# Performance work log

Measured on AMD Instinct MI355X. Metric: run time of the kernel, lower is better.

Reference implementation:

```python
import jax, jax.numpy as jnp
import numpy as np

H = 128          # num_hidden
NUM_IN = 256     # 2*H: h_E (H) + gathered neighbor h_V (H)
SCALE = 30.0
LN_EPS = 1e-5


def _ln(x, g, b):
    mu = jnp.mean(x, axis=-1, keepdims=True)
    var = jnp.mean((x - mu) ** 2, axis=-1, keepdims=True)
    return (x - mu) * jax.lax.rsqrt(var + LN_EPS) * g + b


def _gather_nodes(nodes, idx):
    # nodes: [B,L,C], idx: [B,L,K] -> [B,L,K,C]
    B = nodes.shape[0]
    return nodes[jnp.arange(B)[:, None, None], idx]


def _mlp3(x, W1, b1, W2, b2, W3, b3):
    h = jax.nn.gelu(x @ W1 + b1, approximate=False)
    h = jax.nn.gelu(h @ W2 + b2, approximate=False)
    return h @ W3 + b3


def setup_inputs() -> dict:
    key = jax.random.key(0)
    ks = jax.random.split(key, 16)
    B, L, K = 2, 2048, 48
    s = 0.02
    inp = {
        "h_V": jax.random.normal(ks[0], (B, L, H), jnp.float32),
        "h_E": jax.random.normal(ks[1], (B, L, K, H), jnp.float32),
        "E_idx": jax.random.randint(ks[2], (B, L, K), 0, L, jnp.int32),
        "mask_V": jnp.ones((B, L), jnp.float32),
        "mask_attend": jnp.ones((B, L, K), jnp.float32),
        # node-update MLP
        "W1": jax.random.normal(ks[3], (H + NUM_IN, H), jnp.float32) * s,
        "b1": jnp.zeros((H,), jnp.float32),
        "W2": jax.random.normal(ks[4], (H, H), jnp.float32) * s,
        "b2": jnp.zeros((H,), jnp.float32),
        "W3": jax.random.normal(ks[5], (H, H), jnp.float32) * s,
        "b3": jnp.zeros((H,), jnp.float32),
        # edge-update MLP
        "W11": jax.random.normal(ks[6], (H + NUM_IN, H), jnp.float32) * s,
        "b11": jnp.zeros((H,), jnp.float32),
        "W12": jax.random.normal(ks[7], (H, H), jnp.float32) * s,
        "b12": jnp.zeros((H,), jnp.float32),
        "W13": jax.random.normal(ks[8], (H, H), jnp.float32) * s,
        "b13": jnp.zeros((H,), jnp.float32),
        # position-wise FFN (H -> 4H -> H)
        "Win": jax.random.normal(ks[9], (H, 4 * H), jnp.float32) * s,
        "bin": jnp.zeros((4 * H,), jnp.float32),
        "Wout": jax.random.normal(ks[10], (4 * H, H), jnp.float32) * s,
        "bout": jnp.zeros((H,), jnp.float32),
        # LayerNorms
        "g1": jnp.ones((H,), jnp.float32), "be1": jnp.zeros((H,), jnp.float32),
        "g2": jnp.ones((H,), jnp.float32), "be2": jnp.zeros((H,), jnp.float32),
        "g3": jnp.ones((H,), jnp.float32), "be3": jnp.zeros((H,), jnp.float32),
    }
    return inp


def reference(h_V, h_E, E_idx, mask_V, mask_attend,
              W1, b1, W2, b2, W3, b3,
              W11, b11, W12, b12, W13, b13,
              Win, bin, Wout, bout,
              g1, be1, g2, be2, g3, be3):
    K = h_E.shape[-2]
    # --- node update: gather, concat, 3-layer MLP, masked mean-sum, LN residual ---
    h_nbr = _gather_nodes(h_V, E_idx)                               # [B,L,K,H]
    h_V_exp = jnp.broadcast_to(h_V[:, :, None, :], h_nbr.shape)     # [B,L,K,H]
    h_EV = jnp.concatenate([h_V_exp, h_E, h_nbr], axis=-1)          # [B,L,K,3H]
    h_msg = _mlp3(h_EV, W1, b1, W2, b2, W3, b3)                     # [B,L,K,H]
    h_msg = mask_attend[..., None] * h_msg
    dh = jnp.sum(h_msg, axis=-2) / SCALE                            # [B,L,H]
    h_V = _ln(h_V + dh, g1, be1)
    # position-wise FFN + LN residual
    dh = jax.nn.gelu(h_V @ Win + bin, approximate=False) @ Wout + bout
    h_V = _ln(h_V + dh, g2, be2)
    h_V = mask_V[..., None] * h_V
    # --- edge update ---
    h_nbr = _gather_nodes(h_V, E_idx)
    h_V_exp = jnp.broadcast_to(h_V[:, :, None, :], h_nbr.shape)
    h_EV = jnp.concatenate([h_V_exp, h_E, h_nbr], axis=-1)
    h_msg = _mlp3(h_EV, W11, b11, W12, b12, W13, b13)
    h_E = _ln(h_E + h_msg, g3, be3)
    return (h_V, h_E)
```

## Files before the change

kernel.cpp:

```cpp
#include <hip/hip_runtime.h>
#include <hip/hip_bf16.h>

typedef __attribute__((ext_vector_type(8))) short short8;
typedef __attribute__((ext_vector_type(4))) float f32x4;

__device__ inline short f2bf(float f) {
    unsigned u = __builtin_bit_cast(unsigned, f);
    u += 0x7fffu + ((u >> 16) & 1u);
    return (short)(u >> 16);
}
__device__ inline float bf2f(short s) {
    return __builtin_bit_cast(float, ((unsigned)(unsigned short)s) << 16);
}
__device__ inline float bflo(unsigned u) { return __builtin_bit_cast(float, u << 16); }
__device__ inline float bfhi(unsigned u) { return __builtin_bit_cast(float, u & 0xffff0000u); }
__device__ inline unsigned cvt_pk_bf16(float a, float b) {
    unsigned r;
    asm("v_cvt_pk_bf16_f32 %0, %1, %2" : "=v"(r) : "v"(a), "v"(b));
    return r;
}
__device__ inline float gelu_fast(float x) {
    float z = x * (1.0f + 0.044715f * x * x);
    float e = __expf(1.5957691216f * z);
    return x - x * __builtin_amdgcn_rcpf(e + 1.0f);
}
__device__ inline float wred(float s) {
#pragma unroll
    for (int o = 32; o; o >>= 1) s += __shfl_xor(s, o, 64);
    return s;
}

__global__ void pack_all_kernel(const float* __restrict__ W1, const float* __restrict__ W2,
                                const float* __restrict__ W3, const float* __restrict__ W11,
                                const float* __restrict__ W12, const float* __restrict__ W13,
                                const float* __restrict__ Win, const float* __restrict__ Wout,
                                short* __restrict__ out) {
    int b = blockIdx.x;
    if (b < 80) {
        int which = b >> 3;
        const float* Ws[10] = {W1 + 128 * 128, W2, W3, W11 + 128 * 128, W12, W13,
                               W1, W1 + 256 * 128, W11, W11 + 256 * 128};
        const float* W = Ws[which];
        int i = (b & 7) * 256 + threadIdx.x;
        int lane = i & 63, tile = i >> 6;
        int kt = tile & 3, nt = tile >> 2;
        int n = nt * 16 + (lane & 15);
        int k0 = kt * 32 + (lane >> 4) * 8;
        short8 v;
#pragma unroll
        for (int j = 0; j < 8; ++j) v[j] = f2bf(W[(size_t)(k0 + j) * 128 + n]);
        *(short8*)(out + (size_t)which * 16384 + (size_t)i * 8) = v;
    } else if (b < 112) {
        int i = (b - 80) * 256 + threadIdx.x;
        int lane = i & 63, tile = i >> 6;
        int kt = tile & 3, nt = tile >> 2;
        int n = nt * 16 + (lane & 15);
        int k0 = kt * 32 + (lane >> 4) * 8;
        short8 v;
#pragma unroll
        for (int j = 0; j < 8; ++j) v[j] = f2bf(Win[(size_t)(k0 + j) * 512 + n]);
        *(short8*)(out + 163840 + (size_t)i * 8) = v;
    } else {
        int i = (b - 112) * 256 + threadIdx.x;
        int lane = i & 63, tile = i >> 6;
        int kt = tile & 15, nt = tile >> 4;
        int n = nt * 16 + (lane & 15);
        int k0 = kt * 32 + (lane >> 4) * 8;
        short8 v;
#pragma unroll
        for (int j = 0; j < 8; ++j) v[j] = f2bf(Wout[(size_t)(k0 + j) * 128 + n]);
        *(short8*)(out + 229376 + (size_t)i * 8) = v;
    }
}

__global__ __launch_bounds__(256) void node_pre_kernel(
    const float* __restrict__ hV, const short8* __restrict__ Bs,
    const short8* __restrict__ Bn, const float* __restrict__ bias,
    float* __restrict__ Ys, short* __restrict__ Yn) {
    int n0 = blockIdx.x * 16;
    int tid = threadIdx.x, lane = tid & 63, w = tid >> 6;
    __shared__ __align__(16) short A_sw[16 * 128];
    {
        int off = tid * 8;
        int r = off >> 7, c0 = off & 127;
        const float* src = hV + (size_t)n0 * 128 + off;
        float4 f0 = *(const float4*)(src);
        float4 f1 = *(const float4*)(src + 4);
        uint4 u;
        u.x = cvt_pk_bf16(f0.x, f0.y); u.y = cvt_pk_bf16(f0.z, f0.w);
        u.z = cvt_pk_bf16(f1.x, f1.y); u.w = cvt_pk_bf16(f1.z, f1.w);
        *(uint4*)((char*)A_sw + r * 256 + ((c0 * 2) ^ ((r & 7) << 4))) = u;
    }
    __syncthreads();
    const short8* Bp = (w < 2) ? Bs : Bn;
    f32x4 acc[4];
#pragma unroll
    for (int n2 = 0; n2 < 4; ++n2) acc[n2] = (f32x4){0.f, 0.f, 0.f, 0.f};
#pragma unroll
    for (int kt = 0; kt < 4; ++kt) {
        int row = lane & 15;
        int kb = (kt * 32 + (lane >> 4) * 8) * 2;
        short8 a = *(const short8*)((const char*)A_sw + row * 256 + (kb ^ ((row & 7) << 4)));
#pragma unroll
        for (int n2 = 0; n2 < 4; ++n2) {
            int ntl = (w & 1) * 4 + n2;
            short8 bf = Bp[(ntl * 4 + kt) * 64 + lane];
            acc[n2] = __builtin_amdgcn_mfma_f32_16x16x32_bf16(a, bf, acc[n2], 0, 0, 0);
        }
    }
    if (w < 2) {
#pragma unroll
        for (int n2 = 0; n2 < 4; ++n2) {
            int col = ((w & 1) * 4 + n2) * 16 + (lane & 15);
            float bv = bias[col];
#pragma unroll
            for (int i = 0; i < 4; ++i) {
                int row = (lane >> 4) * 4 + i;
                Ys[(size_t)(n0 + row) * 128 + col] = acc[n2][i] + bv;
            }
        }
    } else {
#pragma unroll
        for (int n2 = 0; n2 < 4; ++n2) {
            int col = ((w & 1) * 4 + n2) * 16 + (lane & 15);
#pragma unroll
            for (int i = 0; i < 4; ++i) {
                int row = (lane >> 4) * 4 + i;
                Yn[(size_t)(n0 + row) * 128 + col] = f2bf(acc[n2][i]);
            }
        }
    }
}


__device__ inline void gemm48_a(const short* A_sw, const short8* __restrict__ Wp,
                                int w, int lane, f32x4 acc[3][2]) {
#pragma unroll
    for (int mt = 0; mt < 3; ++mt)
#pragma unroll
        for (int n2 = 0; n2 < 2; ++n2) acc[mt][n2] = (f32x4){0.f, 0.f, 0.f, 0.f};
#pragma unroll
    for (int kt = 0; kt < 4; ++kt) {
        short8 a[3];
        int kb = (kt * 32 + (lane >> 4) * 8) * 2;
#pragma unroll
        for (int mt = 0; mt < 3; ++mt) {
            int row = mt * 16 + (lane & 15);
            a[mt] = *(const short8*)((const char*)A_sw + row * 256 + (kb ^ ((row & 7) << 4)));
        }
#pragma unroll
        for (int n2 = 0; n2 < 2; ++n2) {
            short8 bf = Wp[((w * 2 + n2) * 4 + kt) * 64 + lane];
#pragma unroll
            for (int mt = 0; mt < 3; ++mt)
                acc[mt][n2] = __builtin_amdgcn_mfma_f32_16x16x32_bf16(a[mt], bf, acc[mt][n2], 0, 0, 0);
        }
    }
}

__device__ inline void gemm48_swz(const short* A_sw, const short8* __restrict__ Wp,
                                  int w, int lane, f32x4 acc[2][3]) {
#pragma unroll
    for (int m2 = 0; m2 < 2; ++m2)
#pragma unroll
        for (int nt = 0; nt < 3; ++nt) acc[m2][nt] = (f32x4){0.f, 0.f, 0.f, 0.f};
#pragma unroll
    for (int kt = 0; kt < 4; ++kt) {
        int kb = (kt * 32 + (lane >> 4) * 8) * 2;
        short8 e[3];
#pragma unroll
        for (int nt = 0; nt < 3; ++nt) {
            int row = nt * 16 + (lane & 15);
            e[nt] = *(const short8*)((const char*)A_sw + row * 256 + (kb ^ ((row & 7) << 4)));
        }
#pragma unroll
        for (int m2 = 0; m2 < 2; ++m2) {
            short8 wf = Wp[((w * 2 + m2) * 4 + kt) * 64 + lane];
#pragma unroll
            for (int nt = 0; nt < 3; ++nt)
                acc[m2][nt] = __builtin_amdgcn_mfma_f32_16x16x32_bf16(wf, e[nt], acc[m2][nt], 0, 0, 0);
        }
    }
}

__device__ inline void stage_hE(const float* __restrict__ Eb, short* A_sw, int tid) {
#pragma unroll
    for (int i = 0; i < 3; ++i) {
        int e = tid + i * 256;
        int r = e >> 4, c0 = (e & 15) * 8;
        float4 f0 = *(const float4*)(Eb + r * 128 + c0);
        float4 f1 = *(const float4*)(Eb + r * 128 + c0 + 4);
        uint4 u;
        u.x = cvt_pk_bf16(f0.x, f0.y); u.y = cvt_pk_bf16(f0.z, f0.w);
        u.z = cvt_pk_bf16(f1.x, f1.y); u.w = cvt_pk_bf16(f1.z, f1.w);
        *(uint4*)((char*)A_sw + r * 256 + ((c0 * 2) ^ ((r & 7) << 4))) = u;
    }
}

__device__ inline void epi_l1_reg(f32x4 acc[2][3], const float4 ysv[2],
                                  const uint2 ynv[3][2], short* A_sw, int w, int lane) {
#pragma unroll
    for (int m2 = 0; m2 < 2; ++m2) {
        int featb = (w * 2 + m2) * 16 + ((lane >> 4) << 2);
#pragma unroll
        for (int nt = 0; nt < 3; ++nt) {
            int edge = nt * 16 + (lane & 15);
            uint2 yv = ynv[nt][m2];
            float v0 = gelu_fast(acc[m2][nt][0] + ysv[m2].x + bflo(yv.x));
            float v1 = gelu_fast(acc[m2][nt][1] + ysv[m2].y + bfhi(yv.x));
            float v2 = gelu_fast(acc[m2][nt][2] + ysv[m2].z + bflo(yv.y));
            float v3 = gelu_fast(acc[m2][nt][3] + ysv[m2].w + bfhi(yv.y));
            uint2 pk = {cvt_pk_bf16(v0, v1), cvt_pk_bf16(v2, v3)};
            *(uint2*)((char*)A_sw + edge * 256 + ((featb * 2) ^ ((edge & 7) << 4))) = pk;
        }
    }
}

__device__ inline void epi_l2(f32x4 acc[2][3], const float* __restrict__ b,
                              short* A_sw, int w, int lane) {
#pragma unroll
    for (int m2 = 0; m2 < 2; ++m2) {
        int featb = (w * 2 + m2) * 16 + ((lane >> 4) << 2);
        float b0 = b[featb], b1 = b[featb + 1], b2v = b[featb + 2], b3v = b[featb + 3];
#pragma unroll
        for (int nt = 0; nt < 3; ++nt) {
            int edge = nt * 16 + (lane & 15);
            float v0 = gelu_fast(acc[m2][nt][0] + b0);
            float v1 = gelu_fast(acc[m2][nt][1] + b1);
            float v2 = gelu_fast(acc[m2][nt][2] + b2v);
            float v3 = gelu_fast(acc[m2][nt][3] + b3v);
            uint2 pk = {cvt_pk_bf16(v0, v1), cvt_pk_bf16(v2, v3)};
            *(uint2*)((char*)A_sw + edge * 256 + ((featb * 2) ^ ((edge & 7) << 4))) = pk;
        }
    }
}

__global__ __launch_bounds__(256) void node_msg_kernel(
    const float* __restrict__ hV, const float* __restrict__ hE,
    const int* __restrict__ Eidx, const float* __restrict__ maskAtt,
    const short8* __restrict__ W1bp, const short8* __restrict__ W2p,
    const short8* __restrict__ W3p, const float* __restrict__ b2,
    const float* __restrict__ b3, const float* __restrict__ Ysg,
    const short* __restrict__ Yng, const float* __restrict__ g1,
    const float* __restrict__ be1, float* __restrict__ hv1out) {
    const int node = blockIdx.x;
    const int bb = node >> 11;
    const int tid = threadIdx.x;
    const int lane = tid & 63, w = tid >> 6;

    __shared__ __align__(16) short A_sw[48 * 128];
    __shared__ float mask_s[48];
    __shared__ float red[8];

    const int e0 = lane & 15;
    int featb0 = (w * 2) * 16 + ((lane >> 4) << 2);
    int featb1 = featb0 + 16;
    uint2 ynv[3][2];
    float4 ysv[2];
    {
        int i0 = Eidx[node * 48 + e0];
        int i1 = Eidx[node * 48 + 16 + e0];
        int i2 = Eidx[node * 48 + 32 + e0];
        const short* Y0 = Yng + ((size_t)bb * 2048 + i0) * 128;
        const short* Y1 = Yng + ((size_t)bb * 2048 + i1) * 128;
        const short* Y2 = Yng + ((size_t)bb * 2048 + i2) * 128;
        ynv[0][0] = *(const uint2*)(Y0 + featb0); ynv[0][1] = *(const uint2*)(Y0 + featb1);
        ynv[1][0] = *(const uint2*)(Y1 + featb0); ynv[1][1] = *(const uint2*)(Y1 + featb1);
        ynv[2][0] = *(const uint2*)(Y2 + featb0); ynv[2][1] = *(const uint2*)(Y2 + featb1);
        ysv[0] = *(const float4*)(Ysg + (size_t)node * 128 + featb0);
        ysv[1] = *(const float4*)(Ysg + (size_t)node * 128 + featb1);
    }
    stage_hE(hE + (size_t)node * 6144, A_sw, tid);
    if (tid < 48) mask_s[tid] = maskAtt[node * 48 + tid];
    __syncthreads();

    f32x4 acc[2][3];
    gemm48_swz(A_sw, W1bp, w, lane, acc);
    __syncthreads();
    epi_l1_reg(acc, ysv, ynv, A_sw, w, lane);
    __syncthreads();
    gemm48_swz(A_sw, W2p, w, lane, acc);
    __syncthreads();
    epi_l2(acc, b2, A_sw, w, lane);
    __syncthreads();

    f32x4 acc3[3][2];
    gemm48_a(A_sw, W3p, w, lane, acc3);
    float u[2];
#pragma unroll
    for (int n2 = 0; n2 < 2; ++n2) {
        int col = (w * 2 + n2) * 16 + (lane & 15);
        float b3c = b3[col];
        float s = 0.f;
#pragma unroll
        for (int mt = 0; mt < 3; ++mt)
#pragma unroll
            for (int i = 0; i < 4; ++i) {
                int row = mt * 16 + (lane >> 4) * 4 + i;
                s += (acc3[mt][n2][i] + b3c) * mask_s[row];
            }
        s += __shfl_xor(s, 16, 64);
        s += __shfl_xor(s, 32, 64);
        u[n2] = hV[(size_t)node * 128 + col] + s * (1.0f / 30.0f);
    }
    float ps = wred(u[0] + u[1]) * 0.25f;
    float pq = wred(u[0] * u[0] + u[1] * u[1]) * 0.25f;
    if (lane == 0) { red[w] = ps; red[4 + w] = pq; }
    __syncthreads();
    float S = red[0] + red[1] + red[2] + red[3];
    float Q = red[4] + red[5] + red[6] + red[7];
    float mu = S * (1.0f / 128.0f);
    float var = Q * (1.0f / 128.0f) - mu * mu;
    float rs = rsqrtf(var + 1e-5f);
    if ((lane >> 4) == 0) {
#pragma unroll
        for (int n2 = 0; n2 < 2; ++n2) {
            int col = (w * 2 + n2) * 16 + (lane & 15);
            hv1out[(size_t)node * 128 + col] = (u[n2] - mu) * rs * g1[col] + be1[col];
        }
    }
}

__global__ __launch_bounds__(256) void ffn_kernel(
    const float* __restrict__ hv1, const short8* __restrict__ Winp,
    const float* __restrict__ binp, const short8* __restrict__ Woutp,
    const float* __restrict__ bout, const float* __restrict__ g2,
    const float* __restrict__ be2, const float* __restrict__ maskV,
    float* __restrict__ hVout) {
    int n0 = blockIdx.x * 16;
    int tid = threadIdx.x, lane = tid & 63, w = tid >> 6;
    __shared__ float X[16 * 128];
    __shared__ __align__(16) short A_sw[16 * 128];
    __shared__ __align__(16) short H_sw[16 * 512];

    {
        int off = tid * 8;
        int r = off >> 7, c0 = off & 127;
        const float* src = hv1 + (size_t)n0 * 128 + off;
        float4 f0 = *(const float4*)(src);
        float4 f1 = *(const float4*)(src + 4);
        *(float4*)(&X[off]) = f0;
        *(float4*)(&X[off + 4]) = f1;
        uint4 u;
        u.x = cvt_pk_bf16(f0.x, f0.y); u.y = cvt_pk_bf16(f0.z, f0.w);
        u.z = cvt_pk_bf16(f1.x, f1.y); u.w = cvt_pk_bf16(f1.z, f1.w);
        *(uint4*)((char*)A_sw + r * 256 + ((c0 * 2) ^ ((r & 7) << 4))) = u;
    }
    __syncthreads();

    f32x4 acc1[8];
#pragma unroll
    for (int n2 = 0; n2 < 8; ++n2) acc1[n2] = (f32x4){0.f, 0.f, 0.f, 0.f};
#pragma unroll
    for (int kt = 0; kt < 4; ++kt) {
        int row = lane & 15;
        int kb = (kt * 32 + (lane >> 4) * 8) * 2;
        short8 a = *(const short8*)((const char*)A_sw + row * 256 + (kb ^ ((row & 7) << 4)));
#pragma unroll
        for (int n2 = 0; n2 < 8; ++n2) {
            short8 bf = Winp[((w * 8 + n2) * 4 + kt) * 64 + lane];
            acc1[n2] = __builtin_amdgcn_mfma_f32_16x16x32_bf16(a, bf, acc1[n2], 0, 0, 0);
        }
    }
#pragma unroll
    for (int n2 = 0; n2 < 8; ++n2) {
        int col = (w * 8 + n2) * 16 + (lane & 15);
        float bv = binp[col];
#pragma unroll
        for (int i = 0; i < 4; ++i) {
            int row = (lane >> 4) * 4 + i;
            float v = gelu_fast(acc1[n2][i] + bv);
            *(short*)((char*)H_sw + row * 1024 + ((col * 2) ^ ((row & 7) << 4))) = f2bf(v);
        }
    }
    __syncthreads();

    f32x4 acc2[2];
    acc2[0] = (f32x4){0.f, 0.f, 0.f, 0.f};
    acc2[1] = (f32x4){0.f, 0.f, 0.f, 0.f};
#pragma unroll
    for (int kt = 0; kt < 16; ++kt) {
        int row = lane & 15;
        int kb = (kt * 32 + (lane >> 4) * 8) * 2;
        short8 a = *(const short8*)((const char*)H_sw + row * 1024 + (kb ^ ((row & 7) << 4)));
#pragma unroll
        for (int n2 = 0; n2 < 2; ++n2) {
            short8 bf = Woutp[((w * 2 + n2) * 16 + kt) * 64 + lane];
            acc2[n2] = __builtin_amdgcn_mfma_f32_16x16x32_bf16(a, bf, acc2[n2], 0, 0, 0);
        }
    }
#pragma unroll
    for (int n2 = 0; n2 < 2; ++n2) {
        int col = (w * 2 + n2) * 16 + (lane & 15);
        float bo = bout[col];
#pragma unroll
        for (int i = 0; i < 4; ++i) {
            int row = (lane >> 4) * 4 + i;
            X[row * 128 + col] += acc2[n2][i] + bo;
        }
    }
    __syncthreads();

#pragma unroll
    for (int p = 0; p < 4; ++p) {
        int r = p * 4 + w;
        float u0 = X[r * 128 + lane], u1 = X[r * 128 + lane + 64];
        float s = wred(u0 + u1);
        float q = wred(u0 * u0 + u1 * u1);
        float mu = s * (1.0f / 128.0f);
        float var = q * (1.0f / 128.0f) - mu * mu;
        float rs = rsqrtf(var + 1e-5f);
        float mv = maskV[n0 + r];
        hVout[(size_t)(n0 + r) * 128 + lane] = mv * ((u0 - mu) * rs * g2[lane] + be2[lane]);
        hVout[(size_t)(n0 + r) * 128 + lane + 64] = mv * ((u1 - mu) * rs * g2[lane + 64] + be2[lane + 64]);
    }
}

__global__ __launch_bounds__(256) void edge_upd_kernel(
    const float* __restrict__ hE, const int* __restrict__ Eidx,
    const short8* __restrict__ W11bp, const short8* __restrict__ W12p,
    const short8* __restrict__ W13p, const float* __restrict__ b12,
    const float* __restrict__ b13, const float* __restrict__ Ysg,
    const short* __restrict__ Yng, const float* __restrict__ g3,
    const float* __restrict__ be3, float* __restrict__ hEout) {
    const int node = blockIdx.x;
    const int bb = node >> 11;
    const int tid = threadIdx.x;
    const int lane = tid & 63, w = tid >> 6;

    __shared__ __align__(16) short A_sw[48 * 128];

    const float* Eb = hE + (size_t)node * 6144;
    const int e0 = lane & 15;
    int featb0 = (w * 2) * 16 + ((lane >> 4) << 2);
    int featb1 = featb0 + 16;
    uint2 ynv[3][2];
    float4 ysv[2];
    {
        int i0 = Eidx[node * 48 + e0];
        int i1 = Eidx[node * 48 + 16 + e0];
        int i2 = Eidx[node * 48 + 32 + e0];
        const short* Y0 = Yng + ((size_t)bb * 2048 + i0) * 128;
        const short* Y1 = Yng + ((size_t)bb * 2048 + i1) * 128;
        const short* Y2 = Yng + ((size_t)bb * 2048 + i2) * 128;
        ynv[0][0] = *(const uint2*)(Y0 + featb0); ynv[0][1] = *(const uint2*)(Y0 + featb1);
        ynv[1][0] = *(const uint2*)(Y1 + featb0); ynv[1][1] = *(const uint2*)(Y1 + featb1);
        ynv[2][0] = *(const uint2*)(Y2 + featb0); ynv[2][1] = *(const uint2*)(Y2 + featb1);
        ysv[0] = *(const float4*)(Ysg + (size_t)node * 128 + featb0);
        ysv[1] = *(const float4*)(Ysg + (size_t)node * 128 + featb1);
    }
    stage_hE(Eb, A_sw, tid);
    __syncthreads();

    f32x4 acc[2][3];
    gemm48_swz(A_sw, W11bp, w, lane, acc);
    __syncthreads();
    epi_l1_reg(acc, ysv, ynv, A_sw, w, lane);
    __syncthreads();
    gemm48_swz(A_sw, W12p, w, lane, acc);
    __syncthreads();
    float4 resv[3][2];
#pragma unroll
    for (int nt = 0; nt < 3; ++nt) {
        int edge = nt * 16 + e0;
        resv[nt][0] = *(const float4*)(Eb + edge * 128 + featb0);
        resv[nt][1] = *(const float4*)(Eb + edge * 128 + featb1);
    }
    float4 b13v0 = *(const float4*)(b13 + featb0);
    float4 b13v1 = *(const float4*)(b13 + featb1);
    epi_l2(acc, b12, A_sw, w, lane);
    __syncthreads();

    gemm48_swz(A_sw, W13p, w, lane, acc);
    __syncthreads();

#pragma unroll
    for (int m2 = 0; m2 < 2; ++m2) {
        float4 bv = m2 ? b13v1 : b13v0;
        int featb = m2 ? featb1 : featb0;
#pragma unroll
        for (int nt = 0; nt < 3; ++nt) {
            int edge = nt * 16 + e0;
            float v0 = acc[m2][nt][0] + bv.x + resv[nt][m2].x;
            float v1 = acc[m2][nt][1] + bv.y + resv[nt][m2].y;
            float v2 = acc[m2][nt][2] + bv.z + resv[nt][m2].z;
            float v3 = acc[m2][nt][3] + bv.w + resv[nt][m2].w;
            uint2 pk = {cvt_pk_bf16(v0, v1), cvt_pk_bf16(v2, v3)};
            *(uint2*)((char*)A_sw + edge * 256 + ((featb * 2) ^ ((edge & 7) << 4))) = pk;
        }
    }
    __syncthreads();

    float* outb = hEout + (size_t)node * 6144;
    float gl0 = g3[lane], gl1 = g3[lane + 64];
    float bl0 = be3[lane], bl1 = be3[lane + 64];
#pragma unroll
    for (int p = 0; p < 12; ++p) {
        int r = p * 4 + w;
        int sw = (r & 7) << 4;
        float u0 = bf2f(*(const short*)((const char*)A_sw + r * 256 + ((2 * lane) ^ sw)));
        float u1 = bf2f(*(const short*)((const char*)A_sw + r * 256 + ((2 * lane + 128) ^ sw)));
        float s = wred(u0 + u1);
        float q = wred(u0 * u0 + u1 * u1);
        float mu = s * (1.0f / 128.0f);
        float var = q * (1.0f / 128.0f) - mu * mu;
        float rs = rsqrtf(var + 1e-5f);
        outb[r * 128 + lane] = (u0 - mu) * rs * gl0 + bl0;
        outb[r * 128 + lane + 64] = (u1 - mu) * rs * gl1 + bl1;
    }
}

extern "C" void kernel_launch(void* const* d_in, const int* in_sizes, int n_in,
                              void* d_out, int out_size, void* d_ws, size_t ws_size,
                              hipStream_t stream) {
    const float* hV      = (const float*)d_in[0];
    const float* hE      = (const float*)d_in[1];
    const int*   Eidx    = (const int*)d_in[2];
    const float* maskV   = (const float*)d_in[3];
    const float* maskAtt = (const float*)d_in[4];
    const float* W1  = (const float*)d_in[5];
    const float* b1  = (const float*)d_in[6];
    const float* W2  = (const float*)d_in[7];
    const float* b2  = (const float*)d_in[8];
    const float* W3  = (const float*)d_in[9];
    const float* b3  = (const float*)d_in[10];
    const float* W11 = (const float*)d_in[11];
    const float* b11 = (const float*)d_in[12];
    const float* W12 = (const float*)d_in[13];
    const float* b12 = (const float*)d_in[14];
    const float* W13 = (const float*)d_in[15];
    const float* b13 = (const float*)d_in[16];
    const float* Win = (const float*)d_in[17];
    const float* binp= (const float*)d_in[18];
    const float* Wout= (const float*)d_in[19];
    const float* bout= (const float*)d_in[20];
    const float* g1  = (const float*)d_in[21];
    const float* be1 = (const float*)d_in[22];
    const float* g2  = (const float*)d_in[23];
    const float* be2 = (const float*)d_in[24];
    const float* g3  = (const float*)d_in[25];
    const float* be3 = (const float*)d_in[26];

    char* ws = (char*)d_ws;
    short* Wpk  = (short*)ws;
    float* Ys   = (float*)(ws + 1048576);
    short* Yn   = (short*)(ws + 1048576 + 2097152);
    float* hv1  = (float*)(ws + 1048576 + 2097152 + 1048576);

    float* hVout = (float*)d_out;
    float* hEout = hVout + 2 * 2048 * 128;

    const int NNODE = 2 * 2048;

    pack_all_kernel<<<144, 256, 0, stream>>>(W1, W2, W3, W11, W12, W13, Win, Wout, Wpk);

    node_pre_kernel<<<NNODE / 16, 256, 0, stream>>>(hV,
        (const short8*)(Wpk + 98304), (const short8*)(Wpk + 114688), b1, Ys, Yn);

    node_msg_kernel<<<NNODE, 256, 0, stream>>>(hV, hE, Eidx, maskAtt,
        (const short8*)(Wpk), (const short8*)(Wpk + 16384), (const short8*)(Wpk + 32768),
        b2, b3, Ys, Yn, g1, be1, hv1);

    ffn_kernel<<<NNODE / 16, 256, 0, stream>>>(hv1,
        (const short8*)(Wpk + 163840), binp, (const short8*)(Wpk + 229376), bout,
        g2, be2, maskV, hVout);

    node_pre_kernel<<<NNODE / 16, 256, 0, stream>>>(hVout,
        (const short8*)(Wpk + 131072), (const short8*)(Wpk + 147456), b11, Ys, Yn);

    edge_upd_kernel<<<NNODE, 256, 0, stream>>>(hE, Eidx,
        (const short8*)(Wpk + 49152), (const short8*)(Wpk + 65536), (const short8*)(Wpk + 81920),
        b12, b13, Ys, Yn, g3, be3, hEout);
}
```

Baseline: 141.4 us.

## Process several nodes per block with double-buffered h_E staging and prefetch

The node message and edge update kernels now handle CHUNK=4 nodes per block instead of one. While the current node's GEMMs run, the next node's h_E tile is loaded into registers and written into a second LDS buffer, and its gathered neighbour rows and mask are prefetched. This is meant to hide global-load latency and spread per-block startup cost over several nodes. In exchange the grid has 4x fewer blocks, LDS use doubles, and each thread holds more registers, which can lower occupancy and latency hiding across blocks.

```diff
diff --git a/kernel.cpp b/kernel.cpp
--- a/kernel.cpp
+++ b/kernel.cpp
@@ -3,6 +3,8 @@
 
 typedef __attribute__((ext_vector_type(8))) short short8;
 typedef __attribute__((ext_vector_type(4))) float f32x4;
+
+#define CHUNK 4
 
 __device__ inline short f2bf(float f) {
     unsigned u = __builtin_bit_cast(unsigned, f);
@@ -183,18 +185,45 @@
     }
 }
 
-__device__ inline void stage_hE(const float* __restrict__ Eb, short* A_sw, int tid) {
+__device__ inline void stage_load(const float* __restrict__ Eb, int tid, float4 f[6]) {
 #pragma unroll
     for (int i = 0; i < 3; ++i) {
         int e = tid + i * 256;
         int r = e >> 4, c0 = (e & 15) * 8;
-        float4 f0 = *(const float4*)(Eb + r * 128 + c0);
-        float4 f1 = *(const float4*)(Eb + r * 128 + c0 + 4);
+        f[2 * i] = *(const float4*)(Eb + r * 128 + c0);
+        f[2 * i + 1] = *(const float4*)(Eb + r * 128 + c0 + 4);
+    }
+}
+__device__ inline void stage_write(const float4 f[6], short* A_sw, int tid) {
+#pragma unroll
+    for (int i = 0; i < 3; ++i) {
+        int e = tid + i * 256;
+        int r = e >> 4, c0 = (e & 15) * 8;
         uint4 u;
-        u.x = cvt_pk_bf16(f0.x, f0.y); u.y = cvt_pk_bf16(f0.z, f0.w);
-        u.z = cvt_pk_bf16(f1.x, f1.y); u.w = cvt_pk_bf16(f1.z, f1.w);
+        u.x = cvt_pk_bf16(f[2 * i].x, f[2 * i].y);
+        u.y = cvt_pk_bf16(f[2 * i].z, f[2 * i].w);
+        u.z = cvt_pk_bf16(f[2 * i + 1].x, f[2 * i + 1].y);
+        u.w = cvt_pk_bf16(f[2 * i + 1].z, f[2 * i + 1].w);
         *(uint4*)((char*)A_sw + r * 256 + ((c0 * 2) ^ ((r & 7) << 4))) = u;
     }
+}
+
+__device__ inline void prefetch_yn_ys(const short* __restrict__ Yng,
+                                      const float* __restrict__ Ysg,
+                                      const int* __restrict__ Eidx,
+                                      int node, int bb, int e0, int featb0, int featb1,
+                                      uint2 ynv[3][2], float4 ysv[2]) {
+    int i0 = Eidx[node * 48 + e0];
+    int i1 = Eidx[node * 48 + 16 + e0];
+    int i2 = Eidx[node * 48 + 32 + e0];
+    const short* Y0 = Yng + ((size_t)bb * 2048 + i0) * 128;
+    const short* Y1 = Yng + ((size_t)bb * 2048 + i1) * 128;
+    const short* Y2 = Yng + ((size_t)bb * 2048 + i2) * 128;
+    ynv[0][0] = *(const uint2*)(Y0 + featb0); ynv[0][1] = *(const uint2*)(Y0 + featb1);
+    ynv[1][0] = *(const uint2*)(Y1 + featb0); ynv[1][1] = *(const uint2*)(Y1 + featb1);
+    ynv[2][0] = *(const uint2*)(Y2 + featb0); ynv[2][1] = *(const uint2*)(Y2 + featb1);
+    ysv[0] = *(const float4*)(Ysg + (size_t)node * 128 + featb0);
+    ysv[1] = *(const float4*)(Ysg + (size_t)node * 128 + featb1);
 }
 
 __device__ inline void epi_l1_reg(f32x4 acc[2][3], const float4 ysv[2],
@@ -243,80 +272,92 @@
     const float* __restrict__ b3, const float* __restrict__ Ysg,
     const short* __restrict__ Yng, const float* __restrict__ g1,
     const float* __restrict__ be1, float* __restrict__ hv1out) {
-    const int node = blockIdx.x;
-    const int bb = node >> 11;
+    const int base = blockIdx.x * CHUNK;
+    const int bb = base >> 11;
     const int tid = threadIdx.x;
     const int lane = tid & 63, w = tid >> 6;
 
-    __shared__ __align__(16) short A_sw[48 * 128];
-    __shared__ float mask_s[48];
+    __shared__ __align__(16) short A_sw[2][48 * 128];
+    __shared__ float mask_s[2][48];
     __shared__ float red[8];
 
     const int e0 = lane & 15;
-    int featb0 = (w * 2) * 16 + ((lane >> 4) << 2);
-    int featb1 = featb0 + 16;
-    uint2 ynv[3][2];
-    float4 ysv[2];
-    {
-        int i0 = Eidx[node * 48 + e0];
-        int i1 = Eidx[node * 48 + 16 + e0];
-        int i2 = Eidx[node * 48 + 32 + e0];
-        const short* Y0 = Yng + ((size_t)bb * 2048 + i0) * 128;
-        const short* Y1 = Yng + ((size_t)bb * 2048 + i1) * 128;
-        const short* Y2 = Yng + ((size_t)bb * 2048 + i2) * 128;
-        ynv[0][0] = *(const uint2*)(Y0 + featb0); ynv[0][1] = *(const uint2*)(Y0 + featb1);
-        ynv[1][0] = *(const uint2*)(Y1 + featb0); ynv[1][1] = *(const uint2*)(Y1 + featb1);
-        ynv[2][0] = *(const uint2*)(Y2 + featb0); ynv[2][1] = *(const uint2*)(Y2 + featb1);
-        ysv[0] = *(const float4*)(Ysg + (size_t)node * 128 + featb0);
-        ysv[1] = *(const float4*)(Ysg + (size_t)node * 128 + featb1);
-    }
-    stage_hE(hE + (size_t)node * 6144, A_sw, tid);
-    if (tid < 48) mask_s[tid] = maskAtt[node * 48 + tid];
+    const int featb0 = (w * 2) * 16 + ((lane >> 4) << 2);
+    const int featb1 = featb0 + 16;
+
+    uint2 ynv[3][2], ynv_n[3][2];
+    float4 ysv[2], ysv_n[2];
+    float4 fst[6];
+
+    prefetch_yn_ys(Yng, Ysg, Eidx, base, bb, e0, featb0, featb1, ynv, ysv);
+    stage_load(hE + (size_t)base * 6144, tid, fst);
+    stage_write(fst, A_sw[0], tid);
+    if (tid < 48) mask_s[0][tid] = maskAtt[base * 48 + tid];
     __syncthreads();
 
-    f32x4 acc[2][3];
-    gemm48_swz(A_sw, W1bp, w, lane, acc);
-    __syncthreads();
-    epi_l1_reg(acc, ysv, ynv, A_sw, w, lane);
-    __syncthreads();
-    gemm48_swz(A_sw, W2p, w, lane, acc);
-    __syncthreads();
-    epi_l2(acc, b2, A_sw, w, lane);
-    __syncthreads();
-
-    f32x4 acc3[3][2];
-    gemm48_a(A_sw, W3p, w, lane, acc3);
-    float u[2];
-#pragma unroll
-    for (int n2 = 0; n2 < 2; ++n2) {
-        int col = (w * 2 + n2) * 16 + (lane & 15);
-        float b3c = b3[col];
-        float s = 0.f;
-#pragma unroll
-        for (int mt = 0; mt < 3; ++mt)
-#pragma unroll
-            for (int i = 0; i < 4; ++i) {
-                int row = mt * 16 + (lane >> 4) * 4 + i;
-                s += (acc3[mt][n2][i] + b3c) * mask_s[row];
-            }
-        s += __shfl_xor(s, 16, 64);
-        s += __shfl_xor(s, 32, 64);
-        u[n2] = hV[(size_t)node * 128 + col] + s * (1.0f / 30.0f);
-    }
-    float ps = wred(u[0] + u[1]) * 0.25f;
-    float pq = wred(u[0] * u[0] + u[1] * u[1]) * 0.25f;
-    if (lane == 0) { red[w] = ps; red[4 + w] = pq; }
-    __syncthreads();
-    float S = red[0] + red[1] + red[2] + red[3];
-    float Q = red[4] + red[5] + red[6] + red[7];
-    float mu = S * (1.0f / 128.0f);
-    float var = Q * (1.0f / 128.0f) - mu * mu;
-    float rs = rsqrtf(var + 1e-5f);
-    if ((lane >> 4) == 0) {
+    for (int k = 0; k < CHUNK; ++k) {
+        const int node = base + k;
+        const int p = k & 1;
+        const bool more = (k + 1 < CHUNK);
+
+        if (more) stage_load(hE + (size_t)(node + 1) * 6144, tid, fst);
+
+        f32x4 acc[2][3];
+        gemm48_swz(A_sw[p], W1bp, w, lane, acc);
+        __syncthreads();
+        epi_l1_reg(acc, ysv, ynv, A_sw[p], w, lane);
+        if (more) {
+            prefetch_yn_ys(Yng, Ysg, Eidx, node + 1, bb, e0, featb0, featb1, ynv_n, ysv_n);
+            if (tid < 48) mask_s[p ^ 1][tid] = maskAtt[(node + 1) * 48 + tid];
+        }
+        __syncthreads();
+        gemm48_swz(A_sw[p], W2p, w, lane, acc);
+        __syncthreads();
+        if (more) stage_write(fst, A_sw[p ^ 1], tid);
+        epi_l2(acc, b2, A_sw[p], w, lane);
+        __syncthreads();
+
+        f32x4 acc3[3][2];
+        gemm48_a(A_sw[p], W3p, w, lane, acc3);
+        float u[2];
 #pragma unroll
         for (int n2 = 0; n2 < 2; ++n2) {
             int col = (w * 2 + n2) * 16 + (lane & 15);
-            hv1out[(size_t)node * 128 + col] = (u[n2] - mu) * rs * g1[col] + be1[col];
+            float b3c = b3[col];
+            float s = 0.f;
+#pragma unroll
+            for (int mt = 0; mt < 3; ++mt)
+#pragma unroll
+                for (int i = 0; i < 4; ++i) {
+                    int row = mt * 16 + (lane >> 4) * 4 + i;
+                    s += (acc3[mt][n2][i] + b3c) * mask_s[p][row];
+                }
+            s += __shfl_xor(s, 16, 64);
+            s += __shfl_xor(s, 32, 64);
+            u[n2] = hV[(size_t)node * 128 + col] + s * (1.0f / 30.0f);
+        }
+        float ps = wred(u[0] + u[1]) * 0.25f;
+        float pq = wred(u[0] * u[0] + u[1] * u[1]) * 0.25f;
+        if (lane == 0) { red[w] = ps; red[4 + w] = pq; }
+        __syncthreads();
+        float S = red[0] + red[1] + red[2] + red[3];
+        float Q = red[4] + red[5] + red[6] + red[7];
+        float mu = S * (1.0f / 128.0f);
+        float var = Q * (1.0f / 128.0f) - mu * mu;
+        float rs = rsqrtf(var + 1e-5f);
+        if ((lane >> 4) == 0) {
+#pragma unroll
+            for (int n2 = 0; n2 < 2; ++n2) {
+                int col = (w * 2 + n2) * 16 + (lane & 15);
+                hv1out[(size_t)node * 128 + col] = (u[n2] - mu) * rs * g1[col] + be1[col];
+            }
+        }
+        __syncthreads();
+
+        if (more) {
+#pragma unroll
+            for (int nt = 0; nt < 3; ++nt) { ynv[nt][0] = ynv_n[nt][0]; ynv[nt][1] = ynv_n[nt][1]; }
+            ysv[0] = ysv_n[0]; ysv[1] = ysv_n[1];
         }
     }
 }
@@ -423,90 +464,99 @@
     const float* __restrict__ b13, const float* __restrict__ Ysg,
     const short* __restrict__ Yng, const float* __restrict__ g3,
     const float* __restrict__ be3, float* __restrict__ hEout) {
-    const int node = blockIdx.x;
-    const int bb = node >> 11;
+    const int base = blockIdx.x * CHUNK;
+    const int bb = base >> 11;
     const int tid = threadIdx.x;
     const int lane = tid & 63, w = tid >> 6;
 
-    __shared__ __align__(16) short A_sw[48 * 128];
-
-    const float* Eb = hE + (size_t)node * 6144;
+    __shared__ __align__(16) short A_sw[2][48 * 128];
+
     const int e0 = lane & 15;
-    int featb0 = (w * 2) * 16 + ((lane >> 4) << 2);
-    int featb1 = featb0 + 16;
-    uint2 ynv[3][2];
-    float4 ysv[2];
-    {
-        int i0 = Eidx[node * 48 + e0];
-        int i1 = Eidx[node * 48 + 16 + e0];
-        int i2 = Eidx[node * 48 + 32 + e0];
-        const short* Y0 = Yng + ((size_t)bb * 2048 + i0) * 128;
-        const short* Y1 = Yng + ((size_t)bb * 2048 + i1) * 128;
-        const short* Y2 = Yng + ((size_t)bb * 2048 + i2) * 128;
-        ynv[0][0] = *(const uint2*)(Y0 + featb0); ynv[0][1] = *(const uint2*)(Y0 + featb1);
-        ynv[1][0] = *(const uint2*)(Y1 + featb0); ynv[1][1] = *(const uint2*)(Y1 + featb1);
-        ynv[2][0] = *(const uint2*)(Y2 + featb0); ynv[2][1] = *(const uint2*)(Y2 + featb1);
-        ysv[0] = *(const float4*)(Ysg + (size_t)node * 128 + featb0);
-        ysv[1] = *(const float4*)(Ysg + (size_t)node * 128 + featb1);
-    }
-    stage_hE(Eb, A_sw, tid);
+    const int featb0 = (w * 2) * 16 + ((lane >> 4) << 2);
+    const int featb1 = featb0 + 16;
+
+    uint2 ynv[3][2], ynv_n[3][2];
+    float4 ysv[2], ysv_n[2];
+    float4 fst[6];
+
+    prefetch_yn_ys(Yng, Ysg, Eidx, base, bb, e0, featb0, featb1, ynv, ysv);
+    stage_load(hE + (size_t)base * 6144, tid, fst);
+    stage_write(fst, A_sw[0], tid);
     __syncthreads();
 
-    f32x4 acc[2][3];
-    gemm48_swz(A_sw, W11bp, w, lane, acc);
-    __syncthreads();
-    epi_l1_reg(acc, ysv, ynv, A_sw, w, lane);
-    __syncthreads();
-    gemm48_swz(A_sw, W12p, w, lane, acc);
-    __syncthreads();
-    float4 resv[3][2];
-#pragma unroll
-    for (int nt = 0; nt < 3; ++nt) {
-        int edge = nt * 16 + e0;
-        resv[nt][0] = *(const float4*)(Eb + edge * 128 + featb0);
-        resv[nt][1] = *(const float4*)(Eb + edge * 128 + featb1);
-    }
-    float4 b13v0 = *(const float4*)(b13 + featb0);
-    float4 b13v1 = *(const float4*)(b13 + featb1);
-    epi_l2(acc, b12, A_sw, w, lane);
-    __syncthreads();
-
-    gemm48_swz(A_sw, W13p, w, lane, acc);
-    __syncthreads();
-
-#pragma unroll
-    for (int m2 = 0; m2 < 2; ++m2) {
-        float4 bv = m2 ? b13v1 : b13v0;
-        int featb = m2 ? featb1 : featb0;
+    for (int k = 0; k < CHUNK; ++k) {
+        const int node = base + k;
+        const int p = k & 1;
+        const bool more = (k + 1 < CHUNK);
+        const float* Eb = hE + (size_t)node * 6144;
+
+        if (more) stage_load(hE + (size_t)(node + 1) * 6144, tid, fst);
+
+        f32x4 acc[2][3];
+        gemm48_swz(A_sw[p], W11bp, w, lane, acc);
+        __syncthreads();
+        epi_l1_reg(acc, ysv, ynv, A_sw[p], w, lane);
+        if (more) prefetch_yn_ys(Yng, Ysg, Eidx, node + 1, bb, e0, featb0, featb1, ynv_n, ysv_n);
+        __syncthreads();
+        gemm48_swz(A_sw[p], W12p, w, lane, acc);
+        __syncthreads();
+        float4 resv[3][2];
 #pragma unroll
         for (int nt = 0; nt < 3; ++nt) {
             int edge = nt * 16 + e0;
-            float v0 = acc[m2][nt][0] + bv.x + resv[nt][m2].x;
-            float v1 = acc[m2][nt][1] + bv.y + resv[nt][m2].y;
-            float v2 = acc[m2][nt][2] + bv.z + resv[nt][m2].z;
-            float v3 = acc[m2][nt][3] + bv.w + resv[nt][m2].w;
-            uint2 pk = {cvt_pk_bf16(v0, v1), cvt_pk_bf16(v2, v3)};
-            *(uint2*)((char*)A_sw + edge * 256 + ((featb * 2) ^ ((edge & 7) << 4))) = pk;
-        }
-    }
-    __syncthreads();
-
-    float* outb = hEout + (size_t)node * 6144;
-    float gl0 = g3[lane], gl1 = g3[lane + 64];
-    float bl0 = be3[lane], bl1 = be3[lane + 64];
-#pragma unroll
-    for (int p = 0; p < 12; ++p) {
-        int r = p * 4 + w;
-        int sw = (r & 7) << 4;
-        float u0 = bf2f(*(const short*)((const char*)A_sw + r * 256 + ((2 * lane) ^ sw)));
-        float u1 = bf2f(*(const short*)((const char*)A_sw + r * 256 + ((2 * lane + 128) ^ sw)));
-        float s = wred(u0 + u1);
-        float q = wred(u0 * u0 + u1 * u1);
-        float mu = s * (1.0f / 128.0f);
-        float var = q * (1.0f / 128.0f) - mu * mu;
-        float rs = rsqrtf(var + 1e-5f);
-        outb[r * 128 + lane] = (u0 - mu) * rs * gl0 + bl0;
-        outb[r * 128 + lane + 64] = (u1 - mu) * rs * gl1 + bl1;
+            resv[nt][0] = *(const float4*)(Eb + edge * 128 + featb0);
+            resv[nt][1] = *(const float4*)(Eb + edge * 128 + featb1);
+        }
+        float4 b13v0 = *(const float4*)(b13 + featb0);
+        float4 b13v1 = *(const float4*)(b13 + featb1);
+        if (more) stage_write(fst, A_sw[p ^ 1], tid);
+        epi_l2(acc, b12, A_sw[p], w, lane);
+        __syncthreads();
+
+        gemm48_swz(A_sw[p], W13p, w, lane, acc);
+        __syncthreads();
+
+#pragma unroll
+        for (int m2 = 0; m2 < 2; ++m2) {
+            float4 bv = m2 ? b13v1 : b13v0;
+            int featb = m2 ? featb1 : featb0;
+#pragma unroll
+            for (int nt = 0; nt < 3; ++nt) {
+                int edge = nt * 16 + e0;
+                float v0 = acc[m2][nt][0] + bv.x + resv[nt][m2].x;
+                float v1 = acc[m2][nt][1] + bv.y + resv[nt][m2].y;
+                float v2 = acc[m2][nt][2] + bv.z + resv[nt][m2].z;
+                float v3 = acc[m2][nt][3] + bv.w + resv[nt][m2].w;
+                uint2 pk = {cvt_pk_bf16(v0, v1), cvt_pk_bf16(v2, v3)};
+                *(uint2*)((char*)A_sw[p] + edge * 256 + ((featb * 2) ^ ((edge & 7) << 4))) = pk;
+            }
+        }
+        __syncthreads();
+
+        float* outb = hEout + (size_t)node * 6144;
+        float gl0 = g3[lane], gl1 = g3[lane + 64];
+        float bl0 = be3[lane], bl1 = be3[lane + 64];
+#pragma unroll
+        for (int pr = 0; pr < 12; ++pr) {
+            int r = pr * 4 + w;
+            int sw = (r & 7) << 4;
+            float u0 = bf2f(*(const short*)((const char*)A_sw[p] + r * 256 + ((2 * lane) ^ sw)));
+            float u1 = bf2f(*(const short*)((const char*)A_sw[p] + r * 256 + ((2 * lane + 128) ^ sw)));
+            float s = wred(u0 + u1);
+            float q = wred(u0 * u0 + u1 * u1);
+            float mu = s * (1.0f / 128.0f);
+            float var = q * (1.0f / 128.0f) - mu * mu;
+            float rs = rsqrtf(var + 1e-5f);
+            outb[r * 128 + lane] = (u0 - mu) * rs * gl0 + bl0;
+            outb[r * 128 + lane + 64] = (u1 - mu) * rs * gl1 + bl1;
+        }
+        __syncthreads();
+
+        if (more) {
+#pragma unroll
+            for (int nt = 0; nt < 3; ++nt) { ynv[nt][0] = ynv_n[nt][0]; ynv[nt][1] = ynv_n[nt][1]; }
+            ysv[0] = ysv_n[0]; ysv[1] = ysv_n[1];
+        }
     }
 }
 
@@ -557,7 +607,7 @@
     node_pre_kernel<<<NNODE / 16, 256, 0, stream>>>(hV,
         (const short8*)(Wpk + 98304), (const short8*)(Wpk + 114688), b1, Ys, Yn);
 
-    node_msg_kernel<<<NNODE, 256, 0, stream>>>(hV, hE, Eidx, maskAtt,
+    node_msg_kernel<<<NNODE / CHUNK, 256, 0, stream>>>(hV, hE, Eidx, maskAtt,
         (const short8*)(Wpk), (const short8*)(Wpk + 16384), (const short8*)(Wpk + 32768),
         b2, b3, Ys, Yn, g1, be1, hv1);
 
@@ -568,7 +618,7 @@
     node_pre_kernel<<<NNODE / 16, 256, 0, stream>>>(hVout,
         (const short8*)(Wpk + 131072), (const short8*)(Wpk + 147456), b11, Ys, Yn);
 
-    edge_upd_kernel<<<NNODE, 256, 0, stream>>>(hE, Eidx,
+    edge_upd_kernel<<<NNODE / CHUNK, 256, 0, stream>>>(hE, Eidx,
         (const short8*)(Wpk + 49152), (const short8*)(Wpk + 65536), (const short8*)(Wpk + 81920),
         b12, b13, Ys, Yn, g3, be3, hEout);
 }
```

Result: slower. 255.1 us (+80.4%).
